# Kernel optimization log

Measured on AMD Instinct MI355X. Metric: run time of the kernel, lower is better.

Reference implementation:

```python
import jax, jax.numpy as jnp
import numpy as np

N = 65536
APP = 1024
SP = 512
HID = 512
CARD = 16
SUB = HID // CARD  # 32


def setup_inputs() -> dict:
    key = jax.random.key(0)
    ks = jax.random.split(key, 8)
    s1 = 1.0 / np.sqrt(APP)
    s2 = 1.0 / np.sqrt(SP)
    s3 = 1.0 / np.sqrt(SUB)
    return {
        "appearance": jax.random.normal(ks[0], (N, APP), jnp.float32),
        "spatial": jax.random.normal(ks[1], (N, SP), jnp.float32),
        # Batched per-branch weights (torch Linear: y = x @ W.T + b; here stored as [in, out])
        "W1": jax.random.uniform(ks[2], (CARD, APP, SUB), jnp.float32, -s1, s1),
        "b1": jax.random.uniform(ks[3], (CARD, SUB), jnp.float32, -s1, s1),
        "W2": jax.random.uniform(ks[4], (CARD, SP, SUB), jnp.float32, -s2, s2),
        "b2": jax.random.uniform(ks[5], (CARD, SP if False else SUB), jnp.float32, -s2, s2),
        "W3": jax.random.uniform(ks[6], (CARD, SUB, HID), jnp.float32, -s3, s3),
        "b3": jax.random.uniform(ks[7], (CARD, HID), jnp.float32, -s3, s3),
    }


def reference(appearance, spatial, W1, b1, W2, b2, W3, b3):
    # fc1[c] = appearance @ W1[c] + b1[c]; fc2[c] = spatial @ W2[c] + b2[c]
    h1 = jnp.einsum('na,cas->ncs', appearance, W1) + b1[None]  # [N, C, SUB]
    h2 = jnp.einsum('np,cps->ncs', spatial, W2) + b2[None]     # [N, C, SUB]
    h = jax.nn.relu(h1 + h2)
    # sum over branches of (h[:,c] @ W3[c] + b3[c]) == einsum + sum of biases
    out = jnp.einsum('ncs,csh->nh', h, W3) + jnp.sum(b3, axis=0)[None]  # [N, HID]
    return jax.nn.relu(out)
```

## Files before the change

### kernel.cpp

```cpp
#include <hip/hip_runtime.h>

typedef __attribute__((ext_vector_type(4))) float floatx4;
typedef __attribute__((ext_vector_type(8))) short bf16x8;

__device__ __forceinline__ unsigned short f2bf(float f) {
    union { float f; unsigned u; } v; v.f = f;
    unsigned r = v.u + 0x7fffu + ((v.u >> 16) & 1u);
    return (unsigned short)(r >> 16);
}

__global__ void prep_kernel(const float* __restrict__ W1, const float* __restrict__ b1,
                            const float* __restrict__ W2, const float* __restrict__ b2,
                            const float* __restrict__ W3, const float* __restrict__ b3,
                            unsigned short* __restrict__ wcat, unsigned short* __restrict__ w3f,
                            float* __restrict__ bias12, float* __restrict__ bias3s)
{
    int tid = blockIdx.x * 256 + threadIdx.x;
    if (tid < 98304) {
        int l  = tid & 63;
        int nt = (tid >> 6) & 31;
        int kc = tid >> 11;
        int n  = nt * 16 + (l & 15);
        int k0 = kc * 32 + ((l >> 4) << 3);
        int c = n >> 5, s = n & 31;
        union { unsigned short us[8]; int4 v; } pk;
        const float* src = (k0 < 1024) ? (W1 + c * 32768 + k0 * 32 + s)
                                       : (W2 + c * 16384 + (k0 - 1024) * 32 + s);
        #pragma unroll
        for (int j = 0; j < 8; ++j) pk.us[j] = f2bf(src[j * 32]);
        *(int4*)(wcat + (size_t)tid * 8) = pk.v;
    } else if (tid < 131072) {
        int t  = tid - 98304;
        int l  = t & 63;
        int nt = (t >> 6) & 31;
        int kc = t >> 11;
        int n  = nt * 16 + (l & 15);
        int k0 = kc * 32 + ((l >> 4) << 3);
        union { unsigned short us[8]; int4 v; } pk;
        const float* src = W3 + k0 * 512 + n;
        #pragma unroll
        for (int j = 0; j < 8; ++j) pk.us[j] = f2bf(src[j * 512]);
        *(int4*)(w3f + (size_t)t * 8) = pk.v;
    } else if (tid < 131584) {
        int n = tid - 131072;
        bias12[n] = b1[n] + b2[n];
        float sacc = 0.f;
        #pragma unroll
        for (int c = 0; c < 16; ++c) sacc += b3[c * 512 + n];
        bias3s[n] = sacc;
    }
}

__global__ __launch_bounds__(1024, 4) void fused_main(
    const float* __restrict__ app, const float* __restrict__ sp,
    const unsigned short* __restrict__ wcat, const unsigned short* __restrict__ w3f,
    const float* __restrict__ bias12, const float* __restrict__ bias3s,
    float* __restrict__ out)
{
    __shared__ union {
        unsigned short As[2][2][8][64][8];
        unsigned short Hf[8][16][64][8];
    } sh;

    const int tid = (int)threadIdx.x;
    const int w   = tid >> 6;
    const int wm  = w >> 3;
    const int wn  = w & 7;
    const int l   = tid & 63;
    const int rowbase = (int)blockIdx.x * 128;

    const int sr = tid >> 3;
    const int kq = tid & 7;
    const float* appsrc = app + (size_t)(rowbase + sr) * 1024 + kq * 8;
    const float* spsrc  = sp  + (size_t)(rowbase + sr) * 512  + kq * 8;

    const int halfw = kq >> 2, mttw = sr >> 4;
    const int Lw    = ((kq & 3) << 4) + (sr & 15);
    const int roww  = Lw >> 3, slotw = Lw & 7;
    const int wroff = halfw * 8192 + mttw * 1024 + roww * 128 + ((slotw ^ roww) << 4);
    char* shb = (char*)&sh;
    unsigned short* as0 = (unsigned short*)(shb + wroff);
    unsigned short* as1 = (unsigned short*)(shb + 16384 + wroff);

    const int rdoff = ((l >> 3) << 7) + (((l & 7) ^ (l >> 3)) << 4);
    #define AS_RD(buf, half, mt) \
        (*(const bf16x8*)(shb + (buf) * 16384 + (half) * 8192 + \
                          (wm * 4 + (mt)) * 1024 + rdoff))

    floatx4 acc[4][4];
    #pragma unroll
    for (int mt = 0; mt < 4; ++mt)
        #pragma unroll
        for (int nt = 0; nt < 4; ++nt)
            acc[mt][nt] = (floatx4){0.f, 0.f, 0.f, 0.f};

    const unsigned short* wbase = wcat + (size_t)wn * 2048 + (size_t)l * 8;

    bf16x8 bcur[8];
    #pragma unroll
    for (int i = 0; i < 8; ++i)
        bcur[i] = *(const bf16x8*)(wbase + (i >> 2) * 16384 + (i & 3) * 512);
    {
        float4 q0 = *(const float4*)(appsrc);
        float4 q1 = *(const float4*)(appsrc + 4);
        union { unsigned short us[8]; int4 v; } pk;
        pk.us[0] = f2bf(q0.x); pk.us[1] = f2bf(q0.y); pk.us[2] = f2bf(q0.z); pk.us[3] = f2bf(q0.w);
        pk.us[4] = f2bf(q1.x); pk.us[5] = f2bf(q1.y); pk.us[6] = f2bf(q1.z); pk.us[7] = f2bf(q1.w);
        *(int4*)as0 = pk.v;
    }
    float4 pA0 = *(const float4*)(appsrc + 64);
    float4 pA1 = *(const float4*)(appsrc + 68);
    asm volatile("s_waitcnt lgkmcnt(0)" ::: "memory");
    __builtin_amdgcn_s_barrier();

    for (int p = 0; p < 24; ++p) {
        const int buf = p & 1;

        if (p + 1 < 24) {
            union { unsigned short us[8]; int4 v; } pk;
            pk.us[0] = f2bf(pA0.x); pk.us[1] = f2bf(pA0.y); pk.us[2] = f2bf(pA0.z); pk.us[3] = f2bf(pA0.w);
            pk.us[4] = f2bf(pA1.x); pk.us[5] = f2bf(pA1.y); pk.us[6] = f2bf(pA1.z); pk.us[7] = f2bf(pA1.w);
            *(int4*)((buf == 0) ? as1 : as0) = pk.v;
        }

        bf16x8 af[4];
        #pragma unroll
        for (int mt = 0; mt < 4; ++mt)
            af[mt] = AS_RD(buf, 0, mt);
        __builtin_amdgcn_s_setprio(1);
        #pragma unroll
        for (int mt = 0; mt < 4; ++mt)
            #pragma unroll
            for (int nt = 0; nt < 4; ++nt)
                acc[mt][nt] = __builtin_amdgcn_mfma_f32_16x16x32_bf16(
                    af[mt], bcur[nt], acc[mt][nt], 0, 0, 0);
        __builtin_amdgcn_s_setprio(0);

        if (p + 2 < 24) {
            const int c = p + 2;
            const float* src = (c < 16) ? (appsrc + c * 64) : (spsrc + (c - 16) * 64);
            pA0 = *(const float4*)src;
            pA1 = *(const float4*)(src + 4);
        }

        #pragma unroll
        for (int mt = 0; mt < 4; ++mt)
            af[mt] = AS_RD(buf, 1, mt);
        __builtin_amdgcn_s_setprio(1);
        #pragma unroll
        for (int mt = 0; mt < 4; ++mt)
            #pragma unroll
            for (int nt = 0; nt < 4; ++nt)
                acc[mt][nt] = __builtin_amdgcn_mfma_f32_16x16x32_bf16(
                    af[mt], bcur[4 + nt], acc[mt][nt], 0, 0, 0);
        __builtin_amdgcn_s_setprio(0);

        if (p + 1 < 24) {
            const unsigned short* wp = wbase + (size_t)(p + 1) * 32768;
            #pragma unroll
            for (int i = 0; i < 8; ++i)
                bcur[i] = *(const bf16x8*)(wp + (i >> 2) * 16384 + (i & 3) * 512);
        }

        asm volatile("s_waitcnt lgkmcnt(0)" ::: "memory");
        __builtin_amdgcn_s_barrier();
    }

    const unsigned short* w3base = w3f + (size_t)wn * 2048 + (size_t)l * 8;
    bf16x8 b3[8];
    #pragma unroll
    for (int i = 0; i < 8; ++i)
        b3[i] = *(const bf16x8*)(w3base + (i >> 2) * 16384 + (i & 3) * 512);

    #pragma unroll
    for (int nt = 0; nt < 4; ++nt) {
        const int colg = wn * 64 + nt * 16 + (l & 15);
        const float bv = bias12[colg];
        const int kc  = colg >> 5;
        const int lhi = ((colg >> 3) & 3) << 4;
        const int j   = colg & 7;
        #pragma unroll
        for (int mt = 0; mt < 4; ++mt)
            #pragma unroll
            for (int r = 0; r < 4; ++r) {
                const int rlow = ((l >> 4) << 2) + r;
                float v = acc[mt][nt][r] + bv;
                v = fmaxf(v, 0.f);
                sh.Hf[wm * 4 + mt][kc][lhi + rlow][j] = f2bf(v);
            }
    }
    asm volatile("s_waitcnt lgkmcnt(0)" ::: "memory");
    __builtin_amdgcn_s_barrier();

    #pragma unroll
    for (int mt = 0; mt < 4; ++mt)
        #pragma unroll
        for (int nt = 0; nt < 4; ++nt)
            acc[mt][nt] = (floatx4){0.f, 0.f, 0.f, 0.f};

    for (int q = 0; q < 8; ++q) {
        bf16x8 af[4];
        #pragma unroll
        for (int mt = 0; mt < 4; ++mt)
            af[mt] = *(const bf16x8*)(&sh.Hf[wm * 4 + mt][2 * q][l][0]);
        __builtin_amdgcn_s_setprio(1);
        #pragma unroll
        for (int mt = 0; mt < 4; ++mt)
            #pragma unroll
            for (int nt = 0; nt < 4; ++nt)
                acc[mt][nt] = __builtin_amdgcn_mfma_f32_16x16x32_bf16(
                    af[mt], b3[nt], acc[mt][nt], 0, 0, 0);
        __builtin_amdgcn_s_setprio(0);
        #pragma unroll
        for (int mt = 0; mt < 4; ++mt)
            af[mt] = *(const bf16x8*)(&sh.Hf[wm * 4 + mt][2 * q + 1][l][0]);
        __builtin_amdgcn_s_setprio(1);
        #pragma unroll
        for (int mt = 0; mt < 4; ++mt)
            #pragma unroll
            for (int nt = 0; nt < 4; ++nt)
                acc[mt][nt] = __builtin_amdgcn_mfma_f32_16x16x32_bf16(
                    af[mt], b3[4 + nt], acc[mt][nt], 0, 0, 0);
        __builtin_amdgcn_s_setprio(0);
        if (q + 1 < 8) {
            const unsigned short* wp = w3base + (size_t)(q + 1) * 32768;
            #pragma unroll
            for (int i = 0; i < 8; ++i)
                b3[i] = *(const bf16x8*)(wp + (i >> 2) * 16384 + (i & 3) * 512);
        }
    }

    #pragma unroll
    for (int nt = 0; nt < 4; ++nt) {
        const int colg = wn * 64 + nt * 16 + (l & 15);
        const float bv = bias3s[colg];
        #pragma unroll
        for (int mt = 0; mt < 4; ++mt)
            #pragma unroll
            for (int r = 0; r < 4; ++r) {
                const int rowg = wm * 64 + mt * 16 + ((l >> 4) << 2) + r;
                float v = acc[mt][nt][r] + bv;
                v = fmaxf(v, 0.f);
                out[(size_t)(rowbase + rowg) * 512 + colg] = v;
            }
    }
    #undef AS_RD
}

extern "C" void kernel_launch(void* const* d_in, const int* in_sizes, int n_in,
                              void* d_out, int out_size, void* d_ws, size_t ws_size,
                              hipStream_t stream)
{
    const float* app = (const float*)d_in[0];
    const float* sp  = (const float*)d_in[1];
    const float* W1  = (const float*)d_in[2];
    const float* b1  = (const float*)d_in[3];
    const float* W2  = (const float*)d_in[4];
    const float* b2  = (const float*)d_in[5];
    const float* W3  = (const float*)d_in[6];
    const float* b3  = (const float*)d_in[7];

    char* ws = (char*)d_ws;
    unsigned short* wcat  = (unsigned short*)(ws);
    unsigned short* w3f   = (unsigned short*)(ws + 1572864);
    float*          b12   = (float*)(ws + 2097152);
    float*          b3s   = (float*)(ws + 2099200);

    prep_kernel<<<514, 256, 0, stream>>>(W1, b1, W2, b2, W3, b3, wcat, w3f, b12, b3s);

    float* outp = (float*)d_out;
    fused_main<<<65536 / 128, 1024, 0, stream>>>(app, sp, wcat, w3f, b12, b3s, outp);
}
```

Measured before the change: 546.4 us.

## Halve block to 8 waves, doubling per-wave N tile to 64x128

The block shrinks from 16 to 8 waves (2x4), and each wave now computes a 64x128 output tile with 32 accumulators instead of 16. Each thread stages two bf16 chunks of the activation tile per stage. Weight fragments are double-held in two register sets and refilled right after each half's MFMAs. This raises MFMA work per shared-memory A fragment read and cuts the number of waves contending for the barrier, at the cost of much higher VGPR/AGPR pressure and lower occupancy.

Measured after the change: 550.1 us. About the same (+0.7%).

```diff
diff --git a/kernel.cpp b/kernel.cpp
--- a/kernel.cpp
+++ b/kernel.cpp
@@ -51,7 +51,7 @@
     }
 }
 
-__global__ __launch_bounds__(1024, 4) void fused_main(
+__global__ __launch_bounds__(512, 2) void fused_main(
     const float* __restrict__ app, const float* __restrict__ sp,
     const unsigned short* __restrict__ wcat, const unsigned short* __restrict__ w3f,
     const float* __restrict__ bias12, const float* __restrict__ bias3s,
@@ -61,67 +61,80 @@
         unsigned short As[2][2][8][64][8];
         unsigned short Hf[8][16][64][8];
     } sh;
+    char* shb = (char*)&sh;
 
     const int tid = (int)threadIdx.x;
     const int w   = tid >> 6;
-    const int wm  = w >> 3;
-    const int wn  = w & 7;
+    const int wm  = w >> 2;
+    const int wn  = w & 3;
     const int l   = tid & 63;
     const int rowbase = (int)blockIdx.x * 128;
 
-    const int sr = tid >> 3;
-    const int kq = tid & 7;
-    const float* appsrc = app + (size_t)(rowbase + sr) * 1024 + kq * 8;
-    const float* spsrc  = sp  + (size_t)(rowbase + sr) * 512  + kq * 8;
-
-    const int halfw = kq >> 2, mttw = sr >> 4;
-    const int Lw    = ((kq & 3) << 4) + (sr & 15);
-    const int roww  = Lw >> 3, slotw = Lw & 7;
-    const int wroff = halfw * 8192 + mttw * 1024 + roww * 128 + ((slotw ^ roww) << 4);
-    char* shb = (char*)&sh;
-    unsigned short* as0 = (unsigned short*)(shb + wroff);
-    unsigned short* as1 = (unsigned short*)(shb + 16384 + wroff);
+    const int sr = tid >> 2;
+    const int kq = tid & 3;
+    const float* appsrc = app + (size_t)(rowbase + sr) * 1024 + kq * 16;
+    const float* spsrc  = sp  + (size_t)(rowbase + sr) * 512  + kq * 16;
+
+    const int mttw = sr >> 4;
+    const int o0 = 2 * kq, o1 = 2 * kq + 1;
+    const int L0 = (o0 & 3) * 16 + (sr & 15);
+    const int L1 = (o1 & 3) * 16 + (sr & 15);
+    const int wr0 = (o0 >> 2) * 8192 + mttw * 1024 + (L0 >> 3) * 128 + (((L0 & 7) ^ (L0 >> 3)) << 4);
+    const int wr1 = (o1 >> 2) * 8192 + mttw * 1024 + (L1 >> 3) * 128 + (((L1 & 7) ^ (L1 >> 3)) << 4);
 
     const int rdoff = ((l >> 3) << 7) + (((l & 7) ^ (l >> 3)) << 4);
     #define AS_RD(buf, half, mt) \
         (*(const bf16x8*)(shb + (buf) * 16384 + (half) * 8192 + \
                           (wm * 4 + (mt)) * 1024 + rdoff))
 
-    floatx4 acc[4][4];
+    #define STAGE(bb) do {                                                    \
+        union { unsigned short us[8]; int4 v; } pk;                           \
+        pk.us[0] = f2bf(pA0.x); pk.us[1] = f2bf(pA0.y);                       \
+        pk.us[2] = f2bf(pA0.z); pk.us[3] = f2bf(pA0.w);                       \
+        pk.us[4] = f2bf(pA1.x); pk.us[5] = f2bf(pA1.y);                       \
+        pk.us[6] = f2bf(pA1.z); pk.us[7] = f2bf(pA1.w);                       \
+        *(int4*)(shb + (bb) + wr0) = pk.v;                                    \
+        pk.us[0] = f2bf(pA2.x); pk.us[1] = f2bf(pA2.y);                       \
+        pk.us[2] = f2bf(pA2.z); pk.us[3] = f2bf(pA2.w);                       \
+        pk.us[4] = f2bf(pA3.x); pk.us[5] = f2bf(pA3.y);                       \
+        pk.us[6] = f2bf(pA3.z); pk.us[7] = f2bf(pA3.w);                       \
+        *(int4*)(shb + (bb) + wr1) = pk.v;                                    \
+    } while (0)
+
+    floatx4 acc[4][8];
     #pragma unroll
     for (int mt = 0; mt < 4; ++mt)
         #pragma unroll
-        for (int nt = 0; nt < 4; ++nt)
+        for (int nt = 0; nt < 8; ++nt)
             acc[mt][nt] = (floatx4){0.f, 0.f, 0.f, 0.f};
 
-    const unsigned short* wbase = wcat + (size_t)wn * 2048 + (size_t)l * 8;
-
-    bf16x8 bcur[8];
+    const unsigned short* wbase = wcat + (size_t)wn * 4096 + (size_t)l * 8;
+
+    bf16x8 bc0[8], bc1[8];
     #pragma unroll
     for (int i = 0; i < 8; ++i)
-        bcur[i] = *(const bf16x8*)(wbase + (i >> 2) * 16384 + (i & 3) * 512);
-    {
-        float4 q0 = *(const float4*)(appsrc);
-        float4 q1 = *(const float4*)(appsrc + 4);
-        union { unsigned short us[8]; int4 v; } pk;
-        pk.us[0] = f2bf(q0.x); pk.us[1] = f2bf(q0.y); pk.us[2] = f2bf(q0.z); pk.us[3] = f2bf(q0.w);
-        pk.us[4] = f2bf(q1.x); pk.us[5] = f2bf(q1.y); pk.us[6] = f2bf(q1.z); pk.us[7] = f2bf(q1.w);
-        *(int4*)as0 = pk.v;
-    }
-    float4 pA0 = *(const float4*)(appsrc + 64);
-    float4 pA1 = *(const float4*)(appsrc + 68);
+        bc0[i] = *(const bf16x8*)(wbase + i * 512);
+    #pragma unroll
+    for (int i = 0; i < 8; ++i)
+        bc1[i] = *(const bf16x8*)(wbase + 16384 + i * 512);
+    float4 pA0, pA1, pA2, pA3;
+    pA0 = *(const float4*)(appsrc);
+    pA1 = *(const float4*)(appsrc + 4);
+    pA2 = *(const float4*)(appsrc + 8);
+    pA3 = *(const float4*)(appsrc + 12);
+    STAGE(0);
+    pA0 = *(const float4*)(appsrc + 64);
+    pA1 = *(const float4*)(appsrc + 68);
+    pA2 = *(const float4*)(appsrc + 72);
+    pA3 = *(const float4*)(appsrc + 76);
     asm volatile("s_waitcnt lgkmcnt(0)" ::: "memory");
     __builtin_amdgcn_s_barrier();
 
     for (int p = 0; p < 24; ++p) {
         const int buf = p & 1;
 
-        if (p + 1 < 24) {
-            union { unsigned short us[8]; int4 v; } pk;
-            pk.us[0] = f2bf(pA0.x); pk.us[1] = f2bf(pA0.y); pk.us[2] = f2bf(pA0.z); pk.us[3] = f2bf(pA0.w);
-            pk.us[4] = f2bf(pA1.x); pk.us[5] = f2bf(pA1.y); pk.us[6] = f2bf(pA1.z); pk.us[7] = f2bf(pA1.w);
-            *(int4*)((buf == 0) ? as1 : as0) = pk.v;
-        }
+        if (p + 1 < 24)
+            STAGE((buf ^ 1) * 16384);
 
         bf16x8 af[4];
         #pragma unroll
@@ -131,16 +144,24 @@
         #pragma unroll
         for (int mt = 0; mt < 4; ++mt)
             #pragma unroll
-            for (int nt = 0; nt < 4; ++nt)
+            for (int nt = 0; nt < 8; ++nt)
                 acc[mt][nt] = __builtin_amdgcn_mfma_f32_16x16x32_bf16(
-                    af[mt], bcur[nt], acc[mt][nt], 0, 0, 0);
+                    af[mt], bc0[nt], acc[mt][nt], 0, 0, 0);
         __builtin_amdgcn_s_setprio(0);
+        if (p + 1 < 24) {
+            const unsigned short* wp = wbase + (size_t)(2 * (p + 1)) * 16384;
+            #pragma unroll
+            for (int i = 0; i < 8; ++i)
+                bc0[i] = *(const bf16x8*)(wp + i * 512);
+        }
 
         if (p + 2 < 24) {
             const int c = p + 2;
             const float* src = (c < 16) ? (appsrc + c * 64) : (spsrc + (c - 16) * 64);
-            pA0 = *(const float4*)src;
+            pA0 = *(const float4*)(src);
             pA1 = *(const float4*)(src + 4);
+            pA2 = *(const float4*)(src + 8);
+            pA3 = *(const float4*)(src + 12);
         }
 
         #pragma unroll
@@ -150,31 +171,30 @@
         #pragma unroll
         for (int mt = 0; mt < 4; ++mt)
             #pragma unroll
-            for (int nt = 0; nt < 4; ++nt)
+            for (int nt = 0; nt < 8; ++nt)
                 acc[mt][nt] = __builtin_amdgcn_mfma_f32_16x16x32_bf16(
-                    af[mt], bcur[4 + nt], acc[mt][nt], 0, 0, 0);
+                    af[mt], bc1[nt], acc[mt][nt], 0, 0, 0);
         __builtin_amdgcn_s_setprio(0);
-
         if (p + 1 < 24) {
-            const unsigned short* wp = wbase + (size_t)(p + 1) * 32768;
+            const unsigned short* wp = wbase + (size_t)(2 * (p + 1) + 1) * 16384;
             #pragma unroll
             for (int i = 0; i < 8; ++i)
-                bcur[i] = *(const bf16x8*)(wp + (i >> 2) * 16384 + (i & 3) * 512);
+                bc1[i] = *(const bf16x8*)(wp + i * 512);
         }
 
         asm volatile("s_waitcnt lgkmcnt(0)" ::: "memory");
         __builtin_amdgcn_s_barrier();
     }
 
-    const unsigned short* w3base = w3f + (size_t)wn * 2048 + (size_t)l * 8;
+    const unsigned short* w3base = w3f + (size_t)wn * 4096 + (size_t)l * 8;
     bf16x8 b3[8];
     #pragma unroll
     for (int i = 0; i < 8; ++i)
-        b3[i] = *(const bf16x8*)(w3base + (i >> 2) * 16384 + (i & 3) * 512);
-
-    #pragma unroll
-    for (int nt = 0; nt < 4; ++nt) {
-        const int colg = wn * 64 + nt * 16 + (l & 15);
+        b3[i] = *(const bf16x8*)(w3base + i * 512);
+
+    #pragma unroll
+    for (int nt = 0; nt < 8; ++nt) {
+        const int colg = wn * 128 + nt * 16 + (l & 15);
         const float bv = bias12[colg];
         const int kc  = colg >> 5;
         const int lhi = ((colg >> 3) & 3) << 4;
@@ -195,44 +215,33 @@
     #pragma unroll
     for (int mt = 0; mt < 4; ++mt)
         #pragma unroll
-        for (int nt = 0; nt < 4; ++nt)
+        for (int nt = 0; nt < 8; ++nt)
             acc[mt][nt] = (floatx4){0.f, 0.f, 0.f, 0.f};
 
-    for (int q = 0; q < 8; ++q) {
+    for (int kc = 0; kc < 16; ++kc) {
         bf16x8 af[4];
         #pragma unroll
         for (int mt = 0; mt < 4; ++mt)
-            af[mt] = *(const bf16x8*)(&sh.Hf[wm * 4 + mt][2 * q][l][0]);
+            af[mt] = *(const bf16x8*)(&sh.Hf[wm * 4 + mt][kc][l][0]);
         __builtin_amdgcn_s_setprio(1);
         #pragma unroll
         for (int mt = 0; mt < 4; ++mt)
             #pragma unroll
-            for (int nt = 0; nt < 4; ++nt)
+            for (int nt = 0; nt < 8; ++nt)
                 acc[mt][nt] = __builtin_amdgcn_mfma_f32_16x16x32_bf16(
                     af[mt], b3[nt], acc[mt][nt], 0, 0, 0);
         __builtin_amdgcn_s_setprio(0);
-        #pragma unroll
-        for (int mt = 0; mt < 4; ++mt)
-            af[mt] = *(const bf16x8*)(&sh.Hf[wm * 4 + mt][2 * q + 1][l][0]);
-        __builtin_amdgcn_s_setprio(1);
-        #pragma unroll
-        for (int mt = 0; mt < 4; ++mt)
-            #pragma unroll
-            for (int nt = 0; nt < 4; ++nt)
-                acc[mt][nt] = __builtin_amdgcn_mfma_f32_16x16x32_bf16(
-                    af[mt], b3[4 + nt], acc[mt][nt], 0, 0, 0);
-        __builtin_amdgcn_s_setprio(0);
-        if (q + 1 < 8) {
-            const unsigned short* wp = w3base + (size_t)(q + 1) * 32768;
+        if (kc + 1 < 16) {
+            const unsigned short* wp = w3base + (size_t)(kc + 1) * 16384;
             #pragma unroll
             for (int i = 0; i < 8; ++i)
-                b3[i] = *(const bf16x8*)(wp + (i >> 2) * 16384 + (i & 3) * 512);
-        }
-    }
-
-    #pragma unroll
-    for (int nt = 0; nt < 4; ++nt) {
-        const int colg = wn * 64 + nt * 16 + (l & 15);
+                b3[i] = *(const bf16x8*)(wp + i * 512);
+        }
+    }
+
+    #pragma unroll
+    for (int nt = 0; nt < 8; ++nt) {
+        const int colg = wn * 128 + nt * 16 + (l & 15);
         const float bv = bias3s[colg];
         #pragma unroll
         for (int mt = 0; mt < 4; ++mt)
@@ -245,6 +254,7 @@
             }
     }
     #undef AS_RD
+    #undef STAGE
 }
 
 extern "C" void kernel_launch(void* const* d_in, const int* in_sizes, int n_in,
@@ -269,5 +279,5 @@
     prep_kernel<<<514, 256, 0, stream>>>(W1, b1, W2, b2, W3, b3, wcat, w3f, b12, b3s);
 
     float* outp = (float*)d_out;
-    fused_main<<<65536 / 128, 1024, 0, stream>>>(app, sp, wcat, w3f, b12, b3s, outp);
-}
+    fused_main<<<65536 / 128, 512, 0, stream>>>(app, sp, wcat, w3f, b12, b3s, outp);
+}
```
